# Kernel optimization log

Hardware: AMD Instinct MI355X
Metric: run time of the kernel (lower is better)

Reference implementation:

```python
import jax, jax.numpy as jnp
import numpy as np

N_NODES = 4096
IN_F = 128
HEADS = 8
HIDDEN = 8  # out_features // n_heads = 64 // 8
SLOPE = 0.2


def setup_inputs() -> dict:
    key = jax.random.key(0)
    k1, k2, k3, k4, k5 = jax.random.split(key, 5)
    h = jax.random.normal(k1, (N_NODES, IN_F), dtype=jnp.float32)
    # sparse-ish dense adjacency mask with guaranteed self-loops (avoids empty softmax rows)
    adj = jax.random.bernoulli(k2, 0.02, (N_NODES, N_NODES))
    adj = adj | jnp.eye(N_NODES, dtype=bool)
    adj = adj[:, :, None]  # [n, n, 1] as in the torch module
    W = jax.random.normal(k3, (IN_F, HEADS * HIDDEN), dtype=jnp.float32) * 0.1
    a_l = jax.random.normal(k4, (HIDDEN,), dtype=jnp.float32) * 0.1
    a_r = jax.random.normal(k5, (HIDDEN,), dtype=jnp.float32) * 0.1
    return {"h": h, "adj": adj, "W": W, "a_l": a_l, "a_r": a_r}


def reference(h, adj, W, a_l, a_r):
    n = h.shape[0]
    g = (h @ W).reshape(n, HEADS, HIDDEN)            # [n, h, d]
    # attn([g_i || g_j]) = g_i . a_l + g_j . a_r (shared across heads)
    sl = jnp.einsum('nhd,d->nh', g, a_l)             # [n, h]
    sr = jnp.einsum('nhd,d->nh', g, a_r)             # [n, h]
    e = sl[:, None, :] + sr[None, :, :]              # [n, n, h] (i = dst, j = src)
    e = jnp.where(e >= 0, e, SLOPE * e)              # leaky relu
    mask = adj[:, :, 0]                              # [n, n] bool
    e = jnp.where(mask[:, :, None], e, -jnp.inf)
    a = jax.nn.softmax(e, axis=1)                    # softmax over source nodes j
    out = jnp.einsum('ijh,jhf->ihf', a, g)           # [n, h, d]
    return out.reshape(n, HEADS * HIDDEN)            # is_concat=True
```

## Files before the change

kernel.cpp:

```cpp
#include <hip/hip_runtime.h>
#include <hip/hip_bf16.h>
#include <math.h>

#define N_NODES 4096
#define IN_F    128
#define HEADS   8
#define HIDDEN  8
#define OUTD    64
#define SLOPE   0.2f

__global__ void detect_kernel(const void* hraw, const void* adjraw, int* flags) {
    __shared__ int f32flag, byteflag;
    if (threadIdx.x == 0) { f32flag = 0; byteflag = 0; }
    __syncthreads();

    const __hip_bfloat16* hb = (const __hip_bfloat16*)hraw;
    int bad = 0;
    for (int idx = (int)threadIdx.x; idx < 512; idx += 256) {
        float v = __bfloat162float(hb[idx]);
        if (!(fabsf(v) < 1e4f)) bad = 1;
    }
    if (bad) atomicOr(&f32flag, 1);

    const unsigned int* aw = (const unsigned int*)adjraw;
    int big = 0;
    for (int idx = (int)threadIdx.x; idx < 1024; idx += 256) {
        if (aw[idx] > 1u) big = 1;
    }
    if (big) atomicOr(&byteflag, 1);

    __syncthreads();
    if (threadIdx.x == 0) { flags[0] = f32flag; flags[1] = byteflag; }
}

__global__ __launch_bounds__(256) void gemm_kernel(
    const void* __restrict__ hraw, const void* __restrict__ Wraw,
    const void* __restrict__ alraw, const void* __restrict__ arraw,
    const int* __restrict__ flags,
    float* __restrict__ g, float* __restrict__ slArr, float* __restrict__ srArr) {

    __shared__ float lh[4][IN_F];
    __shared__ float lg[4][OUTD];

    const int tid  = threadIdx.x;
    const int n0   = blockIdx.x * 4;
    const int isF32 = flags[0];

    if (isF32) {
        const float* hf = (const float*)hraw;
        for (int idx = tid; idx < 4 * IN_F; idx += 256)
            lh[idx >> 7][idx & 127] = hf[(size_t)(n0 + (idx >> 7)) * IN_F + (idx & 127)];
    } else {
        const __hip_bfloat16* hb = (const __hip_bfloat16*)hraw;
        for (int idx = tid; idx < 4 * IN_F; idx += 256)
            lh[idx >> 7][idx & 127] = __bfloat162float(hb[(size_t)(n0 + (idx >> 7)) * IN_F + (idx & 127)]);
    }
    __syncthreads();

    const int nn = tid >> 6;
    const int c  = tid & 63;
    float acc = 0.f;
    if (isF32) {
        const float* Wf = (const float*)Wraw;
        #pragma unroll 8
        for (int k = 0; k < IN_F; ++k) acc += lh[nn][k] * Wf[k * OUTD + c];
    } else {
        const __hip_bfloat16* Wb = (const __hip_bfloat16*)Wraw;
        #pragma unroll 8
        for (int k = 0; k < IN_F; ++k) acc += lh[nn][k] * __bfloat162float(Wb[k * OUTD + c]);
    }
    g[(size_t)(n0 + nn) * OUTD + c] = acc;
    lg[nn][c] = acc;
    __syncthreads();

    if (tid < 32) {
        const int m  = tid >> 3;
        const int hh = tid & 7;
        float sl = 0.f, sr = 0.f;
        if (isF32) {
            const float* al = (const float*)alraw;
            const float* ar = (const float*)arraw;
            #pragma unroll
            for (int d = 0; d < HIDDEN; ++d) {
                float gv = lg[m][hh * HIDDEN + d];
                sl += gv * al[d]; sr += gv * ar[d];
            }
        } else {
            const __hip_bfloat16* al = (const __hip_bfloat16*)alraw;
            const __hip_bfloat16* ar = (const __hip_bfloat16*)arraw;
            #pragma unroll
            for (int d = 0; d < HIDDEN; ++d) {
                float gv = lg[m][hh * HIDDEN + d];
                sl += gv * __bfloat162float(al[d]); sr += gv * __bfloat162float(ar[d]);
            }
        }
        slArr[(size_t)(n0 + m) * HEADS + hh] = sl;
        srArr[(size_t)(n0 + m) * HEADS + hh] = sr;
    }
}

__global__ __launch_bounds__(256) void attn_kernel(
    const void* __restrict__ adjraw, const int* __restrict__ flags,
    const float* __restrict__ g,
    const float* __restrict__ slArr, const float* __restrict__ srArr,
    void* __restrict__ outraw) {

    const int i   = blockIdx.x;
    const int tid = threadIdx.x;

    __shared__ int   edges[1024];
    __shared__ int   cnt;
    __shared__ float sli[HEADS];
    __shared__ float redo[HEADS][32][HIDDEN];
    __shared__ float redl[HEADS][32];
    __shared__ float Lh[HEADS];

    if (tid == 0) cnt = 0;
    if (tid < HEADS) sli[tid] = slArr[(size_t)i * HEADS + tid];
    __syncthreads();

    if (flags[1]) {
        const unsigned int* arow = (const unsigned int*)adjraw + (size_t)i * (N_NODES / 4);
        #pragma unroll
        for (int it = 0; it < N_NODES / 4 / 256; ++it) {
            int wi = it * 256 + tid;
            unsigned int w = arow[wi];
            if (w) {
                #pragma unroll
                for (int b = 0; b < 4; ++b) {
                    if ((w >> (8 * b)) & 0xFFu) {
                        int pos = atomicAdd(&cnt, 1);
                        if (pos < 1024) edges[pos] = wi * 4 + b;
                    }
                }
            }
        }
    } else {
        const int* arow = (const int*)adjraw + (size_t)i * N_NODES;
        #pragma unroll
        for (int it = 0; it < N_NODES / 256; ++it) {
            int j = it * 256 + tid;
            if (arow[j] != 0) {
                int pos = atomicAdd(&cnt, 1);
                if (pos < 1024) edges[pos] = j;
            }
        }
    }
    __syncthreads();

    const int E    = min(cnt, 1024);
    const int hh   = tid & 7;
    const int slot = tid >> 3;
    const float sl_h = sli[hh];

    float l = 0.f;
    float o[HIDDEN] = {0.f, 0.f, 0.f, 0.f, 0.f, 0.f, 0.f, 0.f};

    for (int base = 0; base < E; base += 32) {
        int e = base + slot;
        if (e < E) {
            int j = edges[e];
            float x = sl_h + srArr[(size_t)j * HEADS + hh];
            x = (x >= 0.f) ? x : SLOPE * x;
            float w = __expf(x);
            l += w;
            const float4* gp = (const float4*)(g + (size_t)j * OUTD + hh * HIDDEN);
            float4 g0 = gp[0], g1 = gp[1];
            o[0] += w * g0.x; o[1] += w * g0.y; o[2] += w * g0.z; o[3] += w * g0.w;
            o[4] += w * g1.x; o[5] += w * g1.y; o[6] += w * g1.z; o[7] += w * g1.w;
        }
    }

    redl[hh][slot] = l;
    #pragma unroll
    for (int d = 0; d < HIDDEN; ++d) redo[hh][slot][d] = o[d];
    __syncthreads();

    if (tid < HEADS) {
        float s = 0.f;
        #pragma unroll 8
        for (int k = 0; k < 32; ++k) s += redl[tid][k];
        Lh[tid] = s;
    }
    __syncthreads();

    if (tid < OUTD) {
        const int h2 = tid >> 3, d2 = tid & 7;
        float s = 0.f;
        #pragma unroll 8
        for (int k = 0; k < 32; ++k) s += redo[h2][k][d2];
        float val = s / Lh[h2];
        if (flags[0]) {
            ((float*)outraw)[(size_t)i * OUTD + tid] = val;
        } else {
            ((__hip_bfloat16*)outraw)[(size_t)i * OUTD + tid] = __float2bfloat16(val);
        }
    }
}

extern "C" void kernel_launch(void* const* d_in, const int* in_sizes, int n_in,
                              void* d_out, int out_size, void* d_ws, size_t ws_size,
                              hipStream_t stream) {
    const void* h   = d_in[0];
    const void* adj = d_in[1];
    const void* W   = d_in[2];
    const void* al  = d_in[3];
    const void* ar  = d_in[4];

    char* ws = (char*)d_ws;
    int*   flags = (int*)ws;
    float* g     = (float*)(ws + 256);
    float* slA   = (float*)(ws + 256 + (size_t)N_NODES * OUTD * 4);
    float* srA   = (float*)(ws + 256 + (size_t)N_NODES * OUTD * 4
                                   + (size_t)N_NODES * HEADS * 4);

    detect_kernel<<<1, 256, 0, stream>>>(h, adj, flags);
    gemm_kernel<<<N_NODES / 4, 256, 0, stream>>>(h, W, al, ar, flags, g, slA, srA);
    attn_kernel<<<N_NODES, 256, 0, stream>>>(adj, flags, g, slA, srA, d_out);
}
```

Measured before the change: 127.5 us.

## Fold dtype detection into kernels, vectorize adjacency loads, use shuffle reductions

```diff
diff --git a/kernel.cpp b/kernel.cpp
--- a/kernel.cpp
+++ b/kernel.cpp
@@ -9,51 +9,36 @@
 #define OUTD    64
 #define SLOPE   0.2f
 
-__global__ void detect_kernel(const void* hraw, const void* adjraw, int* flags) {
-    __shared__ int f32flag, byteflag;
-    if (threadIdx.x == 0) { f32flag = 0; byteflag = 0; }
-    __syncthreads();
-
-    const __hip_bfloat16* hb = (const __hip_bfloat16*)hraw;
-    int bad = 0;
-    for (int idx = (int)threadIdx.x; idx < 512; idx += 256) {
-        float v = __bfloat162float(hb[idx]);
-        if (!(fabsf(v) < 1e4f)) bad = 1;
-    }
-    if (bad) atomicOr(&f32flag, 1);
-
-    const unsigned int* aw = (const unsigned int*)adjraw;
-    int big = 0;
-    for (int idx = (int)threadIdx.x; idx < 1024; idx += 256) {
-        if (aw[idx] > 1u) big = 1;
-    }
-    if (big) atomicOr(&byteflag, 1);
-
-    __syncthreads();
-    if (threadIdx.x == 0) { flags[0] = f32flag; flags[1] = byteflag; }
-}
-
 __global__ __launch_bounds__(256) void gemm_kernel(
     const void* __restrict__ hraw, const void* __restrict__ Wraw,
     const void* __restrict__ alraw, const void* __restrict__ arraw,
-    const int* __restrict__ flags,
+    int* __restrict__ flags,
     float* __restrict__ g, float* __restrict__ slArr, float* __restrict__ srArr) {
 
     __shared__ float lh[4][IN_F];
     __shared__ float lg[4][OUTD];
 
-    const int tid  = threadIdx.x;
-    const int n0   = blockIdx.x * 4;
-    const int isF32 = flags[0];
+    const int tid = threadIdx.x;
+    const int n0  = blockIdx.x * 4;
+
+    const __hip_bfloat16* hb = (const __hip_bfloat16*)hraw;
+    float p0 = __bfloat162float(hb[tid]);
+    float p1 = __bfloat162float(hb[tid + 256]);
+    int bad = (!(fabsf(p0) < 1e4f)) | (!(fabsf(p1) < 1e4f));
+    unsigned long long bm = __ballot(bad);
+    const int isF32 = (bm != 0ULL) ? 1 : 0;
+    if (blockIdx.x == 0 && tid == 0) flags[0] = isF32;
 
     if (isF32) {
-        const float* hf = (const float*)hraw;
-        for (int idx = tid; idx < 4 * IN_F; idx += 256)
-            lh[idx >> 7][idx & 127] = hf[(size_t)(n0 + (idx >> 7)) * IN_F + (idx & 127)];
+        const float2* hf = (const float2*)((const float*)hraw + (size_t)n0 * IN_F);
+        ((float2*)&lh[0][0])[tid] = hf[tid];
     } else {
-        const __hip_bfloat16* hb = (const __hip_bfloat16*)hraw;
-        for (int idx = tid; idx < 4 * IN_F; idx += 256)
-            lh[idx >> 7][idx & 127] = __bfloat162float(hb[(size_t)(n0 + (idx >> 7)) * IN_F + (idx & 127)]);
+        const ushort2* h2 = (const ushort2*)((const __hip_bfloat16*)hraw + (size_t)n0 * IN_F);
+        ushort2 v = h2[tid];
+        float2 f;
+        f.x = __bfloat162float(*(__hip_bfloat16*)&v.x);
+        f.y = __bfloat162float(*(__hip_bfloat16*)&v.y);
+        ((float2*)&lh[0][0])[tid] = f;
     }
     __syncthreads();
 
@@ -110,86 +95,101 @@
 
     __shared__ int   edges[1024];
     __shared__ int   cnt;
-    __shared__ float sli[HEADS];
-    __shared__ float redo[HEADS][32][HIDDEN];
-    __shared__ float redl[HEADS][32];
-    __shared__ float Lh[HEADS];
-
-    if (tid == 0) cnt = 0;
-    if (tid < HEADS) sli[tid] = slArr[(size_t)i * HEADS + tid];
-    __syncthreads();
-
-    if (flags[1]) {
-        const unsigned int* arow = (const unsigned int*)adjraw + (size_t)i * (N_NODES / 4);
-        #pragma unroll
-        for (int it = 0; it < N_NODES / 4 / 256; ++it) {
-            int wi = it * 256 + tid;
-            unsigned int w = arow[wi];
-            if (w) {
+    __shared__ int   byteflag;
+    __shared__ float red[4][HEADS * 9];
+
+    if (tid == 0) { cnt = 0; byteflag = 0; }
+    __syncthreads();
+
+    {
+        const uint4* a4 = (const uint4*)adjraw;
+        uint4 d = a4[tid];
+        if ((d.x | d.y | d.z | d.w) > 1u) atomicOr(&byteflag, 1);
+    }
+    __syncthreads();
+
+    if (byteflag) {
+        const uint4* arow = (const uint4*)((const unsigned char*)adjraw + (size_t)i * N_NODES);
+        uint4 w = arow[tid];
+        unsigned int wc[4] = {w.x, w.y, w.z, w.w};
+        #pragma unroll
+        for (int c = 0; c < 4; ++c) {
+            if (wc[c]) {
                 #pragma unroll
                 for (int b = 0; b < 4; ++b) {
-                    if ((w >> (8 * b)) & 0xFFu) {
-                        int pos = atomicAdd(&cnt, 1);
-                        if (pos < 1024) edges[pos] = wi * 4 + b;
+                    if ((wc[c] >> (8 * b)) & 0xFFu) {
+                        int p = atomicAdd(&cnt, 1);
+                        if (p < 1024) edges[p] = tid * 16 + 4 * c + b;
                     }
                 }
             }
         }
     } else {
-        const int* arow = (const int*)adjraw + (size_t)i * N_NODES;
-        #pragma unroll
-        for (int it = 0; it < N_NODES / 256; ++it) {
-            int j = it * 256 + tid;
-            if (arow[j] != 0) {
-                int pos = atomicAdd(&cnt, 1);
-                if (pos < 1024) edges[pos] = j;
-            }
-        }
-    }
-    __syncthreads();
-
-    const int E    = min(cnt, 1024);
-    const int hh   = tid & 7;
-    const int slot = tid >> 3;
-    const float sl_h = sli[hh];
+        const uint4* arow = (const uint4*)((const int*)adjraw + (size_t)i * N_NODES);
+        uint4 w0 = arow[tid];
+        uint4 w1 = arow[tid + 256];
+        uint4 w2 = arow[tid + 512];
+        uint4 w3 = arow[tid + 768];
+        uint4 ww[4] = {w0, w1, w2, w3};
+        #pragma unroll
+        for (int it = 0; it < 4; ++it) {
+            const int base = it * 1024 + tid * 4;
+            uint4 w = ww[it];
+            if (w.x) { int p = atomicAdd(&cnt, 1); if (p < 1024) edges[p] = base + 0; }
+            if (w.y) { int p = atomicAdd(&cnt, 1); if (p < 1024) edges[p] = base + 1; }
+            if (w.z) { int p = atomicAdd(&cnt, 1); if (p < 1024) edges[p] = base + 2; }
+            if (w.w) { int p = atomicAdd(&cnt, 1); if (p < 1024) edges[p] = base + 3; }
+        }
+    }
+    __syncthreads();
+
+    const int E = min(cnt, 1024);
+
+    const int lane = tid & 63;
+    const int wave = tid >> 6;
+    const int hh   = lane & 7;
+    const int s    = lane >> 3;
+    const int slot = wave * 8 + s;
+
+    const float sl_h = slArr[(size_t)i * HEADS + hh];
 
     float l = 0.f;
     float o[HIDDEN] = {0.f, 0.f, 0.f, 0.f, 0.f, 0.f, 0.f, 0.f};
 
-    for (int base = 0; base < E; base += 32) {
-        int e = base + slot;
-        if (e < E) {
-            int j = edges[e];
-            float x = sl_h + srArr[(size_t)j * HEADS + hh];
-            x = (x >= 0.f) ? x : SLOPE * x;
-            float w = __expf(x);
-            l += w;
-            const float4* gp = (const float4*)(g + (size_t)j * OUTD + hh * HIDDEN);
-            float4 g0 = gp[0], g1 = gp[1];
-            o[0] += w * g0.x; o[1] += w * g0.y; o[2] += w * g0.z; o[3] += w * g0.w;
-            o[4] += w * g1.x; o[5] += w * g1.y; o[6] += w * g1.z; o[7] += w * g1.w;
-        }
-    }
-
-    redl[hh][slot] = l;
+    for (int e = slot; e < E; e += 32) {
+        int j = edges[e];
+        float x = sl_h + srArr[(size_t)j * HEADS + hh];
+        x = (x >= 0.f) ? x : SLOPE * x;
+        float wgt = __expf(x);
+        l += wgt;
+        const float4* gp = (const float4*)(g + (size_t)j * OUTD + hh * HIDDEN);
+        float4 g0 = gp[0], g1 = gp[1];
+        o[0] += wgt * g0.x; o[1] += wgt * g0.y; o[2] += wgt * g0.z; o[3] += wgt * g0.w;
+        o[4] += wgt * g1.x; o[5] += wgt * g1.y; o[6] += wgt * g1.z; o[7] += wgt * g1.w;
+    }
+
     #pragma unroll
-    for (int d = 0; d < HIDDEN; ++d) redo[hh][slot][d] = o[d];
-    __syncthreads();
-
-    if (tid < HEADS) {
-        float s = 0.f;
-        #pragma unroll 8
-        for (int k = 0; k < 32; ++k) s += redl[tid][k];
-        Lh[tid] = s;
+    for (int m = 8; m < 64; m <<= 1) {
+        l += __shfl_xor(l, m, 64);
+        #pragma unroll
+        for (int d = 0; d < HIDDEN; ++d) o[d] += __shfl_xor(o[d], m, 64);
+    }
+    if (s == 0) {
+        red[wave][hh * 9 + 8] = l;
+        #pragma unroll
+        for (int d = 0; d < HIDDEN; ++d) red[wave][hh * 9 + d] = o[d];
     }
     __syncthreads();
 
     if (tid < OUTD) {
         const int h2 = tid >> 3, d2 = tid & 7;
-        float s = 0.f;
-        #pragma unroll 8
-        for (int k = 0; k < 32; ++k) s += redo[h2][k][d2];
-        float val = s / Lh[h2];
+        float os = 0.f, ls = 0.f;
+        #pragma unroll
+        for (int w = 0; w < 4; ++w) {
+            os += red[w][h2 * 9 + d2];
+            ls += red[w][h2 * 9 + 8];
+        }
+        float val = os / ls;
         if (flags[0]) {
             ((float*)outraw)[(size_t)i * OUTD + tid] = val;
         } else {
@@ -214,7 +214,6 @@
     float* srA   = (float*)(ws + 256 + (size_t)N_NODES * OUTD * 4
                                    + (size_t)N_NODES * HEADS * 4);
 
-    detect_kernel<<<1, 256, 0, stream>>>(h, adj, flags);
     gemm_kernel<<<N_NODES / 4, 256, 0, stream>>>(h, W, al, ar, flags, g, slA, srA);
     attn_kernel<<<N_NODES, 256, 0, stream>>>(adj, flags, g, slA, srA, d_out);
 }
```

Result: faster. 113.3 us (-11.2%).
